# Optimization experiments

Measured on AMD Instinct MI355X. Metric: run time of the kernel, lower is better.

Reference implementation:

```python
import jax, jax.numpy as jnp
import numpy as np
from jax import lax

EPS = 1e-5
B, NV, NP, C = 1, 12000, 32, 5
VF = 128            # voxel_feat_dim
OF = 256            # output_feat_dim
D0, H0, W0 = 16, 128, 128


def _bn(x, gamma, beta, axes):
    # training-mode batch norm (biased variance), channel dim broadcasts via gamma/beta shape
    mean = jnp.mean(x, axis=axes, keepdims=True)
    var = jnp.var(x, axis=axes, keepdims=True)
    return (x - mean) * lax.rsqrt(var + EPS) * gamma + beta


def _vfe(x, w, b, gamma, beta):
    # x: (B, NVox, NPts, Cin) -> (B, NVox, Cout); linear -> BN1d over all rows -> relu -> max over points
    y = jnp.einsum('bvpc,co->bvpo', x, w) + b
    Bv, Nv, Pp, Co = y.shape
    y = _bn(y.reshape(Bv * Nv * Pp, Co), gamma, beta, axes=0).reshape(Bv, Nv, Pp, Co)
    y = jax.nn.relu(y)
    return jnp.max(y, axis=2)


def _conv_bn_relu(x, w, b, gamma, beta):
    y = lax.conv_general_dilated(x, w, (2, 2, 2), [(1, 1)] * 3,
                                 dimension_numbers=('NCDHW', 'OIDHW', 'NCDHW'))
    y = y + b[None, :, None, None, None]
    y = _bn(y, gamma[None, :, None, None, None], beta[None, :, None, None, None], axes=(0, 2, 3, 4))
    return jax.nn.relu(y)


def setup_inputs() -> dict:
    key = jax.random.key(0)
    ks = jax.random.split(key, 20)
    vf = VF // 2
    inp = {
        'voxel_features': jax.random.normal(ks[0], (B, NV, NP, C), jnp.float32),
        'voxel_coords': jnp.stack([
            jax.random.randint(ks[1], (B, NV), 0, D0),
            jax.random.randint(ks[2], (B, NV), 0, H0),
            jax.random.randint(ks[3], (B, NV), 0, W0)], axis=-1).astype(jnp.int32),
        'grid_d': D0, 'grid_h': H0, 'grid_w': W0,
        # VFE1: 5 -> 64
        'w1': jax.random.normal(ks[4], (C, vf), jnp.float32) * 0.05,
        'b1': jnp.zeros((vf,), jnp.float32),
        'g1': jnp.ones((vf,), jnp.float32),
        'be1': jnp.zeros((vf,), jnp.float32),
        # VFE2: 64 -> 128
        'w2': jax.random.normal(ks[5], (vf, VF), jnp.float32) * 0.05,
        'b2': jnp.zeros((VF,), jnp.float32),
        'g2': jnp.ones((VF,), jnp.float32),
        'be2': jnp.zeros((VF,), jnp.float32),
        # conv3d stack
        'cw1': jax.random.normal(ks[6], (128, VF, 3, 3, 3), jnp.float32) * 0.02,
        'cb1': jnp.zeros((128,), jnp.float32),
        'cg1': jnp.ones((128,), jnp.float32),
        'cbe1': jnp.zeros((128,), jnp.float32),
        'cw2': jax.random.normal(ks[7], (256, 128, 3, 3, 3), jnp.float32) * 0.02,
        'cb2': jnp.zeros((256,), jnp.float32),
        'cg2': jnp.ones((256,), jnp.float32),
        'cbe2': jnp.zeros((256,), jnp.float32),
        'cw3': jax.random.normal(ks[8], (OF, 256, 3, 3, 3), jnp.float32) * 0.02,
        'cb3': jnp.zeros((OF,), jnp.float32),
        'cg3': jnp.ones((OF,), jnp.float32),
        'cbe3': jnp.zeros((OF,), jnp.float32),
    }
    return inp


def reference(voxel_features, voxel_coords, grid_d, grid_h, grid_w,
              w1, b1, g1, be1, w2, b2, g2, be2,
              cw1, cb1, cg1, cbe1, cw2, cb2, cg2, cbe2, cw3, cb3, cg3, cbe3):
    # VFE1: (B, NV, NP, C) -> (B, NV, 64)
    f = _vfe(voxel_features, w1, b1, g1, be1)
    # VFE2 (repaired: singleton points dim, max over 1 point is identity)
    f = _vfe(f[:, :, None, :], w2, b2, g2, be2)  # (B, NV, 128)

    Bn, Nn, Cf = f.shape
    grid = jnp.zeros((Bn, grid_d, grid_h, grid_w, Cf), f.dtype)
    bidx = jnp.broadcast_to(jnp.arange(Bn)[:, None], (Bn, Nn))
    grid = grid.at[bidx, voxel_coords[..., 0], voxel_coords[..., 1], voxel_coords[..., 2]].set(f)
    grid = jnp.transpose(grid, (0, 4, 1, 2, 3))  # (B, Cf, D, H, W)

    x = _conv_bn_relu(grid, cw1, cb1, cg1, cbe1)
    x = _conv_bn_relu(x, cw2, cb2, cg2, cbe2)
    x = _conv_bn_relu(x, cw3, cb3, cg3, cbe3)
    return x
```

## Files before the change

kernel.cpp:

```cpp
#include <hip/hip_runtime.h>

#define NVOX 12000
#define NPTS 32
#define CIN  5
#define C1   64
#define C2   128
#define GD   16
#define GH   128
#define GW   128
#define SP   (GD*GH*GW)
static constexpr float EPSBN = 1e-5f;

typedef unsigned short ushortT;
typedef __attribute__((ext_vector_type(8))) short bf16x8;
typedef __attribute__((ext_vector_type(4))) float f32x4;

__device__ inline ushortT f2bf(float f) {
    unsigned int x = __float_as_uint(f);
    unsigned int r = (x + 0x7FFFu + ((x >> 16) & 1u)) >> 16;
    return (ushortT)r;
}
__device__ inline float bf2f(ushortT u) { return __uint_as_float(((unsigned int)u) << 16); }

__device__ inline void gload16(const ushortT* g, ushortT* l) {
    __builtin_amdgcn_global_load_lds(
        (const __attribute__((address_space(1))) unsigned int*)g,
        (__attribute__((address_space(3))) unsigned int*)l, 16, 0, 0);
}

#define P1D 18
#define P1H 130
#define P1W 130
#define PSP1 (P1D*P1H*P1W)
#define P2D 10
#define P2H 66
#define P2W 66
#define PSP2 (P2D*P2H*P2W)
#define P3D 6
#define P3H 34
#define P3W 34
#define PSP3 (P3D*P3H*P3W)


__device__ inline void conv_w_one(const float* cw, ushortT* wb, int CI_, int TCO_,
                                  int NS_, int e) {
    int j = e & 7;
    int rest = e >> 3;
    int CHN = TCO_*16;
    int p = rest % CHN; int r = rest / CHN;
    int s = r % NS_;    int cob = r / NS_;
    int col = p >> 4, cp = p & 15;
    int cl = cp ^ (col & 7);
    int tap = (CI_==256) ? (s>>1) : s;
    int cib = (CI_==256) ? ((s&1)*128) : 0;
    int co = cob*TCO_ + col;
    int ci = cib + cl*8 + j;
    wb[e] = f2bf(cw[((size_t)co*CI_ + ci)*27 + tap]);
}

__global__ void prep(const float* __restrict__ x, const float* __restrict__ w1,
                     float* __restrict__ s1sum,
                     const float* __restrict__ cw1, const float* __restrict__ cw2,
                     const float* __restrict__ cw3, ushortT* __restrict__ wb1,
                     ushortT* __restrict__ wb2, ushortT* __restrict__ wb3,
                     const int* __restrict__ coords, int* __restrict__ winner) {
    __shared__ float s_w[CIN*C1];
    __shared__ float s_red[2][4][C1];
    const int blk = blockIdx.x;
    const int t = threadIdx.x;
    if (blk < 960) {
        for (int i = t; i < CIN*C1; i += 256) s_w[i] = w1[i];
        __syncthreads();
        int ch = t & 63, rr = t >> 6;
        float sum = 0.f, sq = 0.f;
        const int NROWS = NVOX * NPTS;
        for (int row = blk*4 + rr; row < NROWS; row += 960*4) {
            const float* xr = x + row*CIN;
            float y = 0.f;
            #pragma unroll
            for (int c = 0; c < CIN; ++c) y += xr[c] * s_w[c*C1 + ch];
            sum += y; sq += y*y;
        }
        s_red[0][rr][ch] = sum; s_red[1][rr][ch] = sq;
        __syncthreads();
        if (rr == 0) {
            sum = s_red[0][0][ch]+s_red[0][1][ch]+s_red[0][2][ch]+s_red[0][3][ch];
            sq  = s_red[1][0][ch]+s_red[1][1][ch]+s_red[1][2][ch]+s_red[1][3][ch];
            atomicAdd(&s1sum[ch], sum);
            atomicAdd(&s1sum[C1+ch], sq);
        }
    } else if (blk < 1984) {
        const int N1 = 442368, N2 = 884736, N3 = 1769472;
        const int total = N1+N2+N3;
        for (int e0 = (blk-960)*256 + t; e0 < total; e0 += 1024*256) {
            if (e0 < N1)         conv_w_one(cw1, wb1, 128, 128, 27, e0);
            else if (e0 < N1+N2) conv_w_one(cw2, wb2, 128, 64,  27, e0-N1);
            else                 conv_w_one(cw3, wb3, 256, 64,  54, e0-N1-N2);
        }
    } else {
        int v = (blk-1984)*256 + t;
        if (v < NVOX) {
            int d = coords[v*3+0], h = coords[v*3+1], w = coords[v*3+2];
            atomicMax(&winner[(d*GH + h)*GW + w], v);
        }
    }
}

__global__ void vfe1_apply(const float* __restrict__ x, const float* __restrict__ w1,
                           const float* __restrict__ sums, const float* __restrict__ g,
                           const float* __restrict__ be, float* __restrict__ f1) {
    __shared__ float s_w[CIN*C1];
    __shared__ float s_x[NPTS*CIN];
    int v = blockIdx.x, t = threadIdx.x;
    for (int i = t; i < CIN*C1; i += 64) s_w[i] = w1[i];
    for (int i = t; i < NPTS*CIN; i += 64) s_x[i] = x[v*NPTS*CIN + i];
    const float invN = 1.f/(NVOX*NPTS);
    float mean = sums[t]*invN;
    float var  = sums[C1+t]*invN - mean*mean;
    float sc = g[t]*rsqrtf(var + EPSBN);
    float sh = be[t] - mean*sc;
    __syncthreads();
    float m = 0.f;
    for (int p = 0; p < NPTS; ++p) {
        float y = 0.f;
        #pragma unroll
        for (int c = 0; c < CIN; ++c) y += s_x[p*CIN+c]*s_w[c*C1+t];
        m = fmaxf(m, y*sc + sh);
    }
    f1[v*C1 + t] = m;
}

__global__ void vfe2_linear(const float* __restrict__ f1, const float* __restrict__ w2,
                            float* __restrict__ y2, float* __restrict__ sums) {
    __shared__ float s_w[C2][68];
    __shared__ float s_f[16*C1];
    int t = threadIdx.x;
    for (int i = t; i < C1*C2; i += 128) {
        int c = i >> 7, o = i & 127;
        s_w[o][c] = w2[i];
    }
    int v0 = blockIdx.x*16;
    for (int i = t; i < 16*C1; i += 128) s_f[i] = f1[v0*C1 + i];
    __syncthreads();
    float sum = 0.f, sq = 0.f;
    for (int vl = 0; vl < 16; ++vl) {
        float y = 0.f;
        #pragma unroll
        for (int c4 = 0; c4 < C1; c4 += 4) {
            float4 f = *(const float4*)&s_f[vl*C1 + c4];
            float4 w = *(const float4*)&s_w[t][c4];
            y += f.x*w.x + f.y*w.y + f.z*w.z + f.w*w.w;
        }
        y2[(v0+vl)*C2 + t] = y;
        sum += y; sq += y*y;
    }
    atomicAdd(&sums[t], sum);
    atomicAdd(&sums[C2+t], sq);
}

__global__ void vfe2_apply_bf16(const float* __restrict__ y2, const float* __restrict__ sums,
                                const float* __restrict__ g, const float* __restrict__ be,
                                ushortT* __restrict__ f2b) {
    __shared__ float s_sc[C2], s_sh[C2];
    int t = threadIdx.x;
    if (t < C2) {
        const float invN = 1.f/NVOX;
        float mean = sums[t]*invN;
        float var  = sums[C2+t]*invN - mean*mean;
        float sc = g[t]*rsqrtf(var + EPSBN);
        s_sc[t] = sc; s_sh[t] = be[t] - mean*sc;
    }
    __syncthreads();
    int i = blockIdx.x*256 + t;
    if (i >= NVOX*C2/4) return;
    const float4 v = *(const float4*)(y2 + (size_t)i*4);
    int c0 = (i*4) & (C2-1);
    ushort4 o;
    o.x = f2bf(fmaxf(0.f, v.x*s_sc[c0+0]+s_sh[c0+0]));
    o.y = f2bf(fmaxf(0.f, v.y*s_sc[c0+1]+s_sh[c0+1]));
    o.z = f2bf(fmaxf(0.f, v.z*s_sc[c0+2]+s_sh[c0+2]));
    o.w = f2bf(fmaxf(0.f, v.w*s_sc[c0+3]+s_sh[c0+3]));
    *(ushort4*)(f2b + (size_t)i*4) = o;
}

__global__ void build_grid_cl(const int* __restrict__ winner, const ushortT* __restrict__ f2b,
                              ushortT* __restrict__ grid) {
    const int total = PSP1*16;
    for (int e = blockIdx.x*256 + threadIdx.x; e < total; e += gridDim.x*256) {
        int pos = e >> 4, ch = e & 15;
        int pz = pos / (P1H*P1W); int rr = pos % (P1H*P1W);
        int py = rr / P1W; int px = rr % P1W;
        unsigned dz = pz-1, dy = py-1, dx = px-1;
        int4 v = {0,0,0,0};
        if (dz < GD && dy < GH && dx < GW) {
            int wn_ = winner[(dz*GH + dy)*GW + dx];
            if (wn_ >= 0) v = *(const int4*)(f2b + (size_t)wn_*C2 + ch*8);
        }
        *(int4*)(grid + ((size_t)pos << 7) + ch*8) = v;
    }
}

template<int CI, int CO, int TILE_CO, int TILE_SP, int THREADS,
         int PD, int PH, int PW, int DO, int HO, int WO,
         int OPH, int OPW, int NS, int NSLICE, bool ATOMIC>
__global__ __launch_bounds__(THREADS, 2) void conv3d_mfma(
        const ushortT* __restrict__ in_p, const ushortT* __restrict__ wb,
        void* __restrict__ outp, float* __restrict__ sums_out) {
    constexpr int NW      = THREADS/64;
    constexpr int WAVES_M = TILE_CO/32;
    constexpr int WAVES_N = NW/WAVES_M;
    constexpr int FRAG_N  = TILE_SP/(WAVES_N*16);
    constexpr int TILE_Y  = TILE_SP/8;
    constexpr int SPB     = NS/NSLICE;
    constexpr int WCH     = TILE_CO*16;

    __shared__ ushortT s_x[2][TILE_SP*128];
    __shared__ ushortT s_w[2][TILE_CO*128];

    constexpr int nbx = WO/8, nby = HO/TILE_Y;
    int b = blockIdx.x;
    const int bx = b % nbx; b /= nbx;
    const int by = b % nby; b /= nby;
    const int bz = b % DO;  b /= DO;
    const int cob   = b % (CO/TILE_CO);
    const int slice = b / (CO/TILE_CO);
    const int co0 = cob*TILE_CO;
    const int oy0 = by*TILE_Y, ox0 = bx*8;
    const int t = threadIdx.x;
    const int lane = t & 63, wid = t >> 6;
    const int lr = lane & 15, lq = lane >> 4;
    const int wm = wid % WAVES_M, wn = wid / WAVES_M;

    size_t xpre[4];
    #pragma unroll
    for (int j = 0; j < 4; ++j) {
        int q = t + j*THREADS;
        int n = q >> 4, cp = q & 15;
        int cl = cp ^ (n & 7);
        int oy = n >> 3, ox = n & 7;
        xpre[j] = (size_t)(((2*bz)*PH + (2*oy0 + 2*oy))*PW + (2*ox0 + 2*ox))*CI + cl*8;
    }
    int aoff[2], axr[2], boff[FRAG_N], bxr[FRAG_N];
    #pragma unroll
    for (int f = 0; f < 2; ++f) {
        int c = wm*32 + f*16 + lr;
        aoff[f] = c*128; axr[f] = c & 7;
    }
    #pragma unroll
    for (int f = 0; f < FRAG_N; ++f) {
        int n = wn*(FRAG_N*16) + f*16 + lr;
        boff[f] = n*128; bxr[f] = n & 7;
    }

    f32x4 acc[2][FRAG_N];
    #pragma unroll
    for (int i = 0; i < 2; ++i)
        #pragma unroll
        for (int j = 0; j < FRAG_N; ++j) acc[i][j] = (f32x4){0.f,0.f,0.f,0.f};

    const int s0 = slice*SPB;

#define STAGE(bufi, s) { \
    const int tap_ = (CI==256) ? ((s)>>1) : (s); \
    const int cib_ = (CI==256) ? (((s)&1)*128) : 0; \
    const int kz_ = tap_/9, ky_ = (tap_/3)%3, kx_ = tap_%3; \
    const ushortT* wsrc_ = wb + ((size_t)(cob*NS + (s)))*(WCH*8); \
    _Pragma("unroll") for (int j = 0; j < 4; ++j) \
        gload16(wsrc_ + (size_t)(t + j*THREADS)*8, &s_w[bufi][(wid*64 + j*THREADS)*8]); \
    const size_t koff_ = (size_t)((kz_*PH + ky_)*PW + kx_)*CI + cib_; \
    _Pragma("unroll") for (int j = 0; j < 4; ++j) \
        gload16(in_p + xpre[j] + koff_, &s_x[bufi][(wid*64 + j*THREADS)*8]); }

#define COMPUTE(bufi) { \
    _Pragma("unroll") for (int ks = 0; ks < 4; ++ks) { \
        int cl_ = ks*4 + lq; \
        bf16x8 a0 = *(const bf16x8*)&s_w[bufi][aoff[0] + ((cl_ ^ axr[0])<<3)]; \
        bf16x8 a1 = *(const bf16x8*)&s_w[bufi][aoff[1] + ((cl_ ^ axr[1])<<3)]; \
        _Pragma("unroll") for (int f = 0; f < FRAG_N; ++f) { \
            bf16x8 bf = *(const bf16x8*)&s_x[bufi][boff[f] + ((cl_ ^ bxr[f])<<3)]; \
            acc[0][f] = __builtin_amdgcn_mfma_f32_16x16x32_bf16(a0, bf, acc[0][f],0,0,0); \
            acc[1][f] = __builtin_amdgcn_mfma_f32_16x16x32_bf16(a1, bf, acc[1][f],0,0,0); } } }

    STAGE(0, s0);
    __syncthreads();
    #pragma unroll
    for (int ph = 0; ph < SPB; ++ph) {
        const int buf = ph & 1;
        if (ph + 1 < SPB) STAGE(buf^1, s0 + ph + 1);
        COMPUTE(buf);
        __syncthreads();
    }
#undef STAGE
#undef COMPUTE

    if constexpr (!ATOMIC) {
        ushortT* out = (ushortT*)outp;
        #pragma unroll
        for (int fm = 0; fm < 2; ++fm)
        #pragma unroll
        for (int fn = 0; fn < FRAG_N; ++fn) {
            int n = wn*(FRAG_N*16) + fn*16 + lr;
            int oy = n >> 3, ox = n & 7;
            int c_ = co0 + wm*32 + fm*16 + lq*4;
            size_t pa = ((size_t)(bz+1)*OPH + (oy0+oy+1))*OPW + (ox0+ox+1);
            ushort4 o;
            o.x = f2bf(acc[fm][fn][0]); o.y = f2bf(acc[fm][fn][1]);
            o.z = f2bf(acc[fm][fn][2]); o.w = f2bf(acc[fm][fn][3]);
            *(ushort4*)(out + pa*CO + c_) = o;
        }
        #pragma unroll
        for (int fm = 0; fm < 2; ++fm) {
            float sv[4], qv[4];
            #pragma unroll
            for (int r = 0; r < 4; ++r) {
                float ssum = 0.f, qsum = 0.f;
                #pragma unroll
                for (int fn = 0; fn < FRAG_N; ++fn) {
                    float a = acc[fm][fn][r]; ssum += a; qsum += a*a;
                }
                #pragma unroll
                for (int m = 1; m < 16; m <<= 1) {
                    ssum += __shfl_xor(ssum, m, 64);
                    qsum += __shfl_xor(qsum, m, 64);
                }
                sv[r] = ssum; qv[r] = qsum;
            }
            if (lr == 0) {
                int c_ = co0 + wm*32 + fm*16 + lq*4;
                #pragma unroll
                for (int r = 0; r < 4; ++r) {
                    atomicAdd(&sums_out[c_+r], sv[r]);
                    atomicAdd(&sums_out[CO + c_+r], qv[r]);
                }
            }
        }
    } else {
        float* out = (float*)outp;
        #pragma unroll
        for (int fm = 0; fm < 2; ++fm)
        #pragma unroll
        for (int fn = 0; fn < FRAG_N; ++fn) {
            int n = wn*(FRAG_N*16) + fn*16 + lr;
            int oy = n >> 3, ox = n & 7;
            int c_ = co0 + wm*32 + fm*16 + lq*4;
            #pragma unroll
            for (int r = 0; r < 4; ++r)
                atomicAdd(&out[((size_t)(c_+r)*DO + bz)*(HO*WO) + (oy0+oy)*WO + ox0+ox],
                          acc[fm][fn][r]);
        }
    }
}

template<int C, int PD, int PH, int PW>
__global__ void bn_apply_pad(ushortT* __restrict__ y, const float* __restrict__ sums,
                             const float* __restrict__ g, const float* __restrict__ be,
                             float invN) {
    constexpr int CH = C/8;
    constexpr int total = PD*PH*PW*CH;
    __shared__ float s_sc[C], s_sh[C];
    for (int c = threadIdx.x; c < C; c += 256) {
        float mean = sums[c]*invN;
        float var  = sums[C+c]*invN - mean*mean;
        float sc = g[c]*rsqrtf(var + EPSBN);
        s_sc[c] = sc; s_sh[c] = be[c] - mean*sc;
    }
    __syncthreads();
    for (int e = blockIdx.x*256 + threadIdx.x; e < total; e += gridDim.x*256) {
        int pos = e / CH;
        int c0 = (e % CH)*8;
        int pz = pos / (PH*PW); int rr = pos % (PH*PW);
        int py = rr / PW; int px = rr % PW;
        if ((unsigned)(pz-1) >= (unsigned)(PD-2) || (unsigned)(py-1) >= (unsigned)(PH-2) ||
            (unsigned)(px-1) >= (unsigned)(PW-2)) continue;
        ushortT* p = y + (size_t)pos*C + c0;
        ushort4 a = *(ushort4*)p, b4 = *(ushort4*)(p+4);
        ushort4 o1, o2;
        o1.x = f2bf(fmaxf(0.f, bf2f(a.x)*s_sc[c0+0]+s_sh[c0+0]));
        o1.y = f2bf(fmaxf(0.f, bf2f(a.y)*s_sc[c0+1]+s_sh[c0+1]));
        o1.z = f2bf(fmaxf(0.f, bf2f(a.z)*s_sc[c0+2]+s_sh[c0+2]));
        o1.w = f2bf(fmaxf(0.f, bf2f(a.w)*s_sc[c0+3]+s_sh[c0+3]));
        o2.x = f2bf(fmaxf(0.f, bf2f(b4.x)*s_sc[c0+4]+s_sh[c0+4]));
        o2.y = f2bf(fmaxf(0.f, bf2f(b4.y)*s_sc[c0+5]+s_sh[c0+5]));
        o2.z = f2bf(fmaxf(0.f, bf2f(b4.z)*s_sc[c0+6]+s_sh[c0+6]));
        o2.w = f2bf(fmaxf(0.f, bf2f(b4.w)*s_sc[c0+7]+s_sh[c0+7]));
        *(ushort4*)p     = o1;
        *(ushort4*)(p+4) = o2;
    }
}

template<int SPL>
__global__ void bn_stats_cmajor(const float* __restrict__ y, const float* __restrict__ g,
                                const float* __restrict__ be, float* __restrict__ ss, int C) {
    __shared__ float s_red[2][256];
    int c = blockIdx.x;
    const float* p = y + (size_t)c*SPL;
    float sum = 0.f, sq = 0.f;
    for (int i = threadIdx.x; i < SPL; i += 256) { float v = p[i]; sum += v; sq += v*v; }
    s_red[0][threadIdx.x] = sum; s_red[1][threadIdx.x] = sq;
    __syncthreads();
    for (int s = 128; s > 0; s >>= 1) {
        if (threadIdx.x < s) {
            s_red[0][threadIdx.x] += s_red[0][threadIdx.x+s];
            s_red[1][threadIdx.x] += s_red[1][threadIdx.x+s];
        }
        __syncthreads();
    }
    if (threadIdx.x == 0) {
        float invN = 1.f/(float)SPL;
        float mean = s_red[0][0]*invN;
        float var  = s_red[1][0]*invN - mean*mean;
        float sc = g[c]*rsqrtf(var + EPSBN);
        ss[c] = sc; ss[C+c] = be[c] - mean*sc;
    }
}

template<int LOGSPL>
__global__ void bn_apply_cmajor(float* __restrict__ y, const float* __restrict__ ss,
                                int C, int total) {
    for (int i = blockIdx.x*blockDim.x + threadIdx.x; i < total; i += gridDim.x*blockDim.x) {
        int c = i >> LOGSPL;
        y[i] = fmaxf(0.f, y[i]*ss[c] + ss[C+c]);
    }
}

extern "C" void kernel_launch(void* const* d_in, const int* in_sizes, int n_in,
                              void* d_out, int out_size, void* d_ws, size_t ws_size,
                              hipStream_t stream) {
    const float* x      = (const float*)d_in[0];
    const int*   coords = (const int*)  d_in[1];
    const float* w1  = (const float*)d_in[5];
    const float* g1  = (const float*)d_in[7];
    const float* be1 = (const float*)d_in[8];
    const float* w2  = (const float*)d_in[9];
    const float* g2  = (const float*)d_in[11];
    const float* be2 = (const float*)d_in[12];
    const float* cw1 = (const float*)d_in[13];
    const float* cg1 = (const float*)d_in[15];
    const float* cbe1= (const float*)d_in[16];
    const float* cw2 = (const float*)d_in[17];
    const float* cg2 = (const float*)d_in[19];
    const float* cbe2= (const float*)d_in[20];
    const float* cw3 = (const float*)d_in[21];
    const float* cg3 = (const float*)d_in[23];
    const float* cbe3= (const float*)d_in[24];
    float* out = (float*)d_out;

    float*   ws     = (float*)d_ws;
    float*   stats  = ws;
    int*     winner = (int*)(ws + 4096);
    float*   f1     = (float*)(winner + SP);
    float*   y2     = f1 + (size_t)NVOX*C1;
    ushortT* f2b    = (ushortT*)(y2 + (size_t)NVOX*C2);
    ushortT* grid   = f2b + (size_t)NVOX*C2;
    ushortT* c1o    = grid + (size_t)PSP1*128;
    ushortT* c2o    = c1o + (size_t)PSP2*128;
    ushortT* wb1    = c2o + (size_t)PSP3*256;
    ushortT* wb2    = wb1 + 442368;
    ushortT* wb3    = wb2 + 884736;

    float* s1sum = stats;
    float* s2sum = stats + 128;
    float* c1sum = stats + 384;
    float* c2sum = stats + 640;
    float* ss3   = stats + 1152;

    hipMemsetAsync(stats, 0, 4096*sizeof(float), stream);
    hipMemsetAsync(winner, 0xFF, SP*sizeof(int), stream);
    hipMemsetAsync(c1o, 0, (size_t)PSP2*128*2, stream);
    hipMemsetAsync(c2o, 0, (size_t)PSP3*256*2, stream);
    hipMemsetAsync(d_out, 0, (size_t)out_size*sizeof(float), stream);

    prep<<<2031, 256, 0, stream>>>(x, w1, s1sum, cw1, cw2, cw3, wb1, wb2, wb3,
                                   coords, winner);
    vfe1_apply<<<NVOX, 64, 0, stream>>>(x, w1, s1sum, g1, be1, f1);
    vfe2_linear<<<NVOX/16, 128, 0, stream>>>(f1, w2, y2, s2sum);
    vfe2_apply_bf16<<<NVOX*C2/4/256, 256, 0, stream>>>(y2, s2sum, g2, be2, f2b);
    build_grid_cl<<<4096, 256, 0, stream>>>(winner, f2b, grid);

    conv3d_mfma<128,128, 128,128,512, P1D,P1H,P1W, 8,64,64, P2H,P2W, 27,1,false>
        <<<8*4*8, 512, 0, stream>>>(grid, wb1, c1o, c1sum);
    bn_apply_pad<128, P2D,P2H,P2W><<<1024, 256, 0, stream>>>(c1o, c1sum, cg1, cbe1,
                                                             1.f/32768.f);
    conv3d_mfma<128,256, 64,64,256, P2D,P2H,P2W, 4,32,32, P3H,P3W, 27,1,false>
        <<<4*4*4*4, 256, 0, stream>>>(c1o, wb2, c2o, c2sum);
    bn_apply_pad<256, P3D,P3H,P3W><<<512, 256, 0, stream>>>(c2o, c2sum, cg2, cbe2,
                                                            1.f/4096.f);
    conv3d_mfma<256,256, 64,64,256, P3D,P3H,P3W, 2,16,16, 1,1, 54,6,true>
        <<<2*2*2*4*6, 256, 0, stream>>>(c2o, wb3, (void*)out, nullptr);

    bn_stats_cmajor<2*16*16><<<256, 256, 0, stream>>>(out, cg3, cbe3, ss3, 256);
    bn_apply_cmajor<9><<<512, 256, 0, stream>>>(out, ss3, 256, 131072);
}
```

Before: 281.8 us.

## Generalize conv MFMA wave tiling, use 256-thread conv1, swizzle blocks, batch VFE1

```diff
diff --git a/kernel.cpp b/kernel.cpp
--- a/kernel.cpp
+++ b/kernel.cpp
@@ -110,24 +110,26 @@
                            const float* __restrict__ sums, const float* __restrict__ g,
                            const float* __restrict__ be, float* __restrict__ f1) {
     __shared__ float s_w[CIN*C1];
-    __shared__ float s_x[NPTS*CIN];
-    int v = blockIdx.x, t = threadIdx.x;
-    for (int i = t; i < CIN*C1; i += 64) s_w[i] = w1[i];
-    for (int i = t; i < NPTS*CIN; i += 64) s_x[i] = x[v*NPTS*CIN + i];
+    __shared__ float s_x[4*NPTS*CIN];
+    int v0 = blockIdx.x*4, t = threadIdx.x;
+    for (int i = t; i < CIN*C1; i += 256) s_w[i] = w1[i];
+    for (int i = t; i < 4*NPTS*CIN; i += 256) s_x[i] = x[(size_t)v0*NPTS*CIN + i];
+    int sub = t >> 6, ch = t & 63;
     const float invN = 1.f/(NVOX*NPTS);
-    float mean = sums[t]*invN;
-    float var  = sums[C1+t]*invN - mean*mean;
-    float sc = g[t]*rsqrtf(var + EPSBN);
-    float sh = be[t] - mean*sc;
+    float mean = sums[ch]*invN;
+    float var  = sums[C1+ch]*invN - mean*mean;
+    float sc = g[ch]*rsqrtf(var + EPSBN);
+    float sh = be[ch] - mean*sc;
     __syncthreads();
     float m = 0.f;
+    const float* xs = s_x + sub*NPTS*CIN;
     for (int p = 0; p < NPTS; ++p) {
         float y = 0.f;
         #pragma unroll
-        for (int c = 0; c < CIN; ++c) y += s_x[p*CIN+c]*s_w[c*C1+t];
+        for (int c = 0; c < CIN; ++c) y += xs[p*CIN+c]*s_w[c*C1+ch];
         m = fmaxf(m, y*sc + sh);
     }
-    f1[v*C1 + t] = m;
+    f1[(v0+sub)*C1 + ch] = m;
 }
 
 __global__ void vfe2_linear(const float* __restrict__ f1, const float* __restrict__ w2,
@@ -201,24 +203,26 @@
 }
 
 template<int CI, int CO, int TILE_CO, int TILE_SP, int THREADS,
+         int WAVES_M, int WAVES_N,
          int PD, int PH, int PW, int DO, int HO, int WO,
          int OPH, int OPW, int NS, int NSLICE, bool ATOMIC>
-__global__ __launch_bounds__(THREADS, 2) void conv3d_mfma(
+__global__ __launch_bounds__(THREADS) void conv3d_mfma(
         const ushortT* __restrict__ in_p, const ushortT* __restrict__ wb,
         void* __restrict__ outp, float* __restrict__ sums_out) {
-    constexpr int NW      = THREADS/64;
-    constexpr int WAVES_M = TILE_CO/32;
-    constexpr int WAVES_N = NW/WAVES_M;
-    constexpr int FRAG_N  = TILE_SP/(WAVES_N*16);
-    constexpr int TILE_Y  = TILE_SP/8;
-    constexpr int SPB     = NS/NSLICE;
-    constexpr int WCH     = TILE_CO*16;
+    constexpr int FRAG_M = TILE_CO/(WAVES_M*16);
+    constexpr int FRAG_N = TILE_SP/(WAVES_N*16);
+    constexpr int TILE_Y = TILE_SP/8;
+    constexpr int SPB    = NS/NSLICE;
+    constexpr int WTAP   = TILE_CO*128;
+    constexpr int XCH    = TILE_SP*16/THREADS;
+    constexpr int WCHN   = TILE_CO*16/THREADS;
 
     __shared__ ushortT s_x[2][TILE_SP*128];
     __shared__ ushortT s_w[2][TILE_CO*128];
 
     constexpr int nbx = WO/8, nby = HO/TILE_Y;
-    int b = blockIdx.x;
+    constexpr int NWG = nbx*nby*DO*(CO/TILE_CO)*NSLICE;
+    int b = (blockIdx.x & 7)*(NWG >> 3) + (blockIdx.x >> 3);
     const int bx = b % nbx; b /= nbx;
     const int by = b % nby; b /= nby;
     const int bz = b % DO;  b /= DO;
@@ -231,19 +235,19 @@
     const int lr = lane & 15, lq = lane >> 4;
     const int wm = wid % WAVES_M, wn = wid / WAVES_M;
 
-    size_t xpre[4];
+    size_t xpre[XCH];
     #pragma unroll
-    for (int j = 0; j < 4; ++j) {
+    for (int j = 0; j < XCH; ++j) {
         int q = t + j*THREADS;
         int n = q >> 4, cp = q & 15;
         int cl = cp ^ (n & 7);
         int oy = n >> 3, ox = n & 7;
         xpre[j] = (size_t)(((2*bz)*PH + (2*oy0 + 2*oy))*PW + (2*ox0 + 2*ox))*CI + cl*8;
     }
-    int aoff[2], axr[2], boff[FRAG_N], bxr[FRAG_N];
+    int aoff[FRAG_M], axr[FRAG_M], boff[FRAG_N], bxr[FRAG_N];
     #pragma unroll
-    for (int f = 0; f < 2; ++f) {
-        int c = wm*32 + f*16 + lr;
+    for (int f = 0; f < FRAG_M; ++f) {
+        int c = wm*(FRAG_M*16) + f*16 + lr;
         aoff[f] = c*128; axr[f] = c & 7;
     }
     #pragma unroll
@@ -252,9 +256,9 @@
         boff[f] = n*128; bxr[f] = n & 7;
     }
 
-    f32x4 acc[2][FRAG_N];
+    f32x4 acc[FRAG_M][FRAG_N];
     #pragma unroll
-    for (int i = 0; i < 2; ++i)
+    for (int i = 0; i < FRAG_M; ++i)
         #pragma unroll
         for (int j = 0; j < FRAG_N; ++j) acc[i][j] = (f32x4){0.f,0.f,0.f,0.f};
 
@@ -264,22 +268,24 @@
     const int tap_ = (CI==256) ? ((s)>>1) : (s); \
     const int cib_ = (CI==256) ? (((s)&1)*128) : 0; \
     const int kz_ = tap_/9, ky_ = (tap_/3)%3, kx_ = tap_%3; \
-    const ushortT* wsrc_ = wb + ((size_t)(cob*NS + (s)))*(WCH*8); \
-    _Pragma("unroll") for (int j = 0; j < 4; ++j) \
+    const ushortT* wsrc_ = wb + ((size_t)(cob*NS + (s)))*WTAP; \
+    _Pragma("unroll") for (int j = 0; j < WCHN; ++j) \
         gload16(wsrc_ + (size_t)(t + j*THREADS)*8, &s_w[bufi][(wid*64 + j*THREADS)*8]); \
     const size_t koff_ = (size_t)((kz_*PH + ky_)*PW + kx_)*CI + cib_; \
-    _Pragma("unroll") for (int j = 0; j < 4; ++j) \
+    _Pragma("unroll") for (int j = 0; j < XCH; ++j) \
         gload16(in_p + xpre[j] + koff_, &s_x[bufi][(wid*64 + j*THREADS)*8]); }
 
 #define COMPUTE(bufi) { \
     _Pragma("unroll") for (int ks = 0; ks < 4; ++ks) { \
         int cl_ = ks*4 + lq; \
-        bf16x8 a0 = *(const bf16x8*)&s_w[bufi][aoff[0] + ((cl_ ^ axr[0])<<3)]; \
-        bf16x8 a1 = *(const bf16x8*)&s_w[bufi][aoff[1] + ((cl_ ^ axr[1])<<3)]; \
-        _Pragma("unroll") for (int f = 0; f < FRAG_N; ++f) { \
-            bf16x8 bf = *(const bf16x8*)&s_x[bufi][boff[f] + ((cl_ ^ bxr[f])<<3)]; \
-            acc[0][f] = __builtin_amdgcn_mfma_f32_16x16x32_bf16(a0, bf, acc[0][f],0,0,0); \
-            acc[1][f] = __builtin_amdgcn_mfma_f32_16x16x32_bf16(a1, bf, acc[1][f],0,0,0); } } }
+        bf16x8 av[FRAG_M], bv[FRAG_N]; \
+        _Pragma("unroll") for (int f = 0; f < FRAG_M; ++f) \
+            av[f] = *(const bf16x8*)&s_w[bufi][aoff[f] + ((cl_ ^ axr[f])<<3)]; \
+        _Pragma("unroll") for (int f = 0; f < FRAG_N; ++f) \
+            bv[f] = *(const bf16x8*)&s_x[bufi][boff[f] + ((cl_ ^ bxr[f])<<3)]; \
+        _Pragma("unroll") for (int i = 0; i < FRAG_M; ++i) \
+        _Pragma("unroll") for (int j = 0; j < FRAG_N; ++j) \
+            acc[i][j] = __builtin_amdgcn_mfma_f32_16x16x32_bf16(av[i], bv[j], acc[i][j],0,0,0); } }
 
     STAGE(0, s0);
     __syncthreads();
@@ -296,12 +302,12 @@
     if constexpr (!ATOMIC) {
         ushortT* out = (ushortT*)outp;
         #pragma unroll
-        for (int fm = 0; fm < 2; ++fm)
+        for (int fm = 0; fm < FRAG_M; ++fm)
         #pragma unroll
         for (int fn = 0; fn < FRAG_N; ++fn) {
             int n = wn*(FRAG_N*16) + fn*16 + lr;
             int oy = n >> 3, ox = n & 7;
-            int c_ = co0 + wm*32 + fm*16 + lq*4;
+            int c_ = co0 + wm*(FRAG_M*16) + fm*16 + lq*4;
             size_t pa = ((size_t)(bz+1)*OPH + (oy0+oy+1))*OPW + (ox0+ox+1);
             ushort4 o;
             o.x = f2bf(acc[fm][fn][0]); o.y = f2bf(acc[fm][fn][1]);
@@ -309,7 +315,7 @@
             *(ushort4*)(out + pa*CO + c_) = o;
         }
         #pragma unroll
-        for (int fm = 0; fm < 2; ++fm) {
+        for (int fm = 0; fm < FRAG_M; ++fm) {
             float sv[4], qv[4];
             #pragma unroll
             for (int r = 0; r < 4; ++r) {
@@ -326,7 +332,7 @@
                 sv[r] = ssum; qv[r] = qsum;
             }
             if (lr == 0) {
-                int c_ = co0 + wm*32 + fm*16 + lq*4;
+                int c_ = co0 + wm*(FRAG_M*16) + fm*16 + lq*4;
                 #pragma unroll
                 for (int r = 0; r < 4; ++r) {
                     atomicAdd(&sums_out[c_+r], sv[r]);
@@ -337,12 +343,12 @@
     } else {
         float* out = (float*)outp;
         #pragma unroll
-        for (int fm = 0; fm < 2; ++fm)
+        for (int fm = 0; fm < FRAG_M; ++fm)
         #pragma unroll
         for (int fn = 0; fn < FRAG_N; ++fn) {
             int n = wn*(FRAG_N*16) + fn*16 + lr;
             int oy = n >> 3, ox = n & 7;
-            int c_ = co0 + wm*32 + fm*16 + lq*4;
+            int c_ = co0 + wm*(FRAG_M*16) + fm*16 + lq*4;
             #pragma unroll
             for (int r = 0; r < 4; ++r)
                 atomicAdd(&out[((size_t)(c_+r)*DO + bz)*(HO*WO) + (oy0+oy)*WO + ox0+ox],
@@ -472,20 +478,20 @@
 
     prep<<<2031, 256, 0, stream>>>(x, w1, s1sum, cw1, cw2, cw3, wb1, wb2, wb3,
                                    coords, winner);
-    vfe1_apply<<<NVOX, 64, 0, stream>>>(x, w1, s1sum, g1, be1, f1);
+    vfe1_apply<<<NVOX/4, 256, 0, stream>>>(x, w1, s1sum, g1, be1, f1);
     vfe2_linear<<<NVOX/16, 128, 0, stream>>>(f1, w2, y2, s2sum);
     vfe2_apply_bf16<<<NVOX*C2/4/256, 256, 0, stream>>>(y2, s2sum, g2, be2, f2b);
     build_grid_cl<<<4096, 256, 0, stream>>>(winner, f2b, grid);
 
-    conv3d_mfma<128,128, 128,128,512, P1D,P1H,P1W, 8,64,64, P2H,P2W, 27,1,false>
-        <<<8*4*8, 512, 0, stream>>>(grid, wb1, c1o, c1sum);
+    conv3d_mfma<128,128, 128,128,256, 2,2, P1D,P1H,P1W, 8,64,64, P2H,P2W, 27,1,false>
+        <<<8*4*8, 256, 0, stream>>>(grid, wb1, c1o, c1sum);
     bn_apply_pad<128, P2D,P2H,P2W><<<1024, 256, 0, stream>>>(c1o, c1sum, cg1, cbe1,
                                                              1.f/32768.f);
-    conv3d_mfma<128,256, 64,64,256, P2D,P2H,P2W, 4,32,32, P3H,P3W, 27,1,false>
+    conv3d_mfma<128,256, 64,64,256, 2,2, P2D,P2H,P2W, 4,32,32, P3H,P3W, 27,1,false>
         <<<4*4*4*4, 256, 0, stream>>>(c1o, wb2, c2o, c2sum);
     bn_apply_pad<256, P3D,P3H,P3W><<<512, 256, 0, stream>>>(c2o, c2sum, cg2, cbe2,
                                                             1.f/4096.f);
-    conv3d_mfma<256,256, 64,64,256, P3D,P3H,P3W, 2,16,16, 1,1, 54,6,true>
+    conv3d_mfma<256,256, 64,64,256, 2,2, P3D,P3H,P3W, 2,16,16, 1,1, 54,6,true>
         <<<2*2*2*4*6, 256, 0, stream>>>(c2o, wb3, (void*)out, nullptr);
 
     bn_stats_cmajor<2*16*16><<<256, 256, 0, stream>>>(out, cg3, cbe3, ss3, 256);
```

Result: slower. 306.1 us (+8.6%).
